# Optimization experiments

Measured on AMD Instinct MI355X. Metric: run time of the kernel, lower is better.

The kernel has to match this reference:

```python
import jax, jax.numpy as jnp
from jax import lax
import numpy as np

# dims
N = 8192        # words in sentence
LMAX = 16       # max chars per word (padded)
WED = 506       # word embedding dim
WHD = 512       # word LSTM hidden (input = WED + CHD = 512)
CED = 6         # char embedding dim
CHD = 6         # char LSTM hidden (hardcoded 6 in original)
WV = 50000      # word vocab
CV = 128        # char vocab
T = 64          # tagset size


def setup_inputs() -> dict:
    key = jax.random.key(0)
    ks = jax.random.split(key, 14)
    s = 0.1
    nrm = lambda k, shp: (jax.random.normal(k, shp, dtype=jnp.float32) * s)
    return {
        "sentence_words": jax.random.randint(ks[0], (N,), 0, WV),
        "sentence_characters": jax.random.randint(ks[1], (N, LMAX), 0, CV),
        "char_lengths": jax.random.randint(ks[2], (N,), 1, LMAX + 1),
        "word_emb": nrm(ks[3], (WV, WED)),
        "char_emb": nrm(ks[4], (CV, CED)),
        # PyTorch LSTM gate order: i, f, g, o. b = b_ih + b_hh combined.
        "c_Wih": nrm(ks[5], (4 * CHD, CED)),
        "c_Whh": nrm(ks[6], (4 * CHD, CHD)),
        "c_b": nrm(ks[7], (4 * CHD,)),
        "w_Wih": nrm(ks[8], (4 * WHD, WED + CHD)),
        "w_Whh": nrm(ks[9], (4 * WHD, WHD)),
        "w_b": nrm(ks[10], (4 * WHD,)),
        "out_W": nrm(ks[11], (T, WHD)),
        "out_b": nrm(ks[12], (T,)),
    }


def _gates(pre, c_prev):
    i, f, g, o = jnp.split(pre, 4, axis=-1)
    i = jax.nn.sigmoid(i)
    f = jax.nn.sigmoid(f)
    g = jnp.tanh(g)
    o = jax.nn.sigmoid(o)
    c_new = f * c_prev + i * g
    h_new = o * jnp.tanh(c_new)
    return h_new, c_new


def reference(sentence_words, sentence_characters, char_lengths,
              word_emb, char_emb, c_Wih, c_Whh, c_b,
              w_Wih, w_Whh, w_b, out_W, out_b):
    # ---- char-level LSTM: all words batched, masked by length ----
    ce = char_emb[sentence_characters]                  # [N, LMAX, CED]
    xproj = jnp.einsum('nlc,gc->nlg', ce, c_Wih) + c_b  # [N, LMAX, 4*CHD]
    xproj_t = jnp.swapaxes(xproj, 0, 1)                 # [LMAX, N, 4*CHD]
    mask_t = (jnp.arange(LMAX)[:, None] < char_lengths[None, :])[..., None]  # [LMAX, N, 1]

    def char_step(carry, xm):
        h, c = carry
        xp, m = xm
        h_new, c_new = _gates(xp + h @ c_Whh.T, c)
        return (jnp.where(m, h_new, h), jnp.where(m, c_new, c)), None

    z = jnp.zeros((N, CHD), dtype=xproj.dtype)
    (h_char, _), _ = lax.scan(char_step, (z, z), (xproj_t, mask_t))  # [N, CHD]

    # ---- word-level LSTM over the sentence (batch = 1) ----
    we = word_emb[sentence_words]                       # [N, WED]
    x = jnp.concatenate([we, h_char], axis=1)           # [N, WED+CHD]
    xp = x @ w_Wih.T + w_b                              # [N, 4*WHD]

    def word_step(carry, xt):
        h, c = carry
        h_new, c_new = _gates(xt + h @ w_Whh.T, c)
        return (h_new, c_new), h_new

    zw = jnp.zeros((WHD,), dtype=xp.dtype)
    _, hs = lax.scan(word_step, (zw, zw), xp)           # [N, WHD]

    logits = hs @ out_W.T + out_b                       # [N, T]
    return jax.nn.log_softmax(logits, axis=1)
```

## Files before the change

### kernel.cpp

```cpp
#include <hip/hip_runtime.h>
#include <hip/hip_bf16.h>
#include <math.h>

#define N_WORDS 8192
#define LMAX    16
#define WED     506
#define WHD     512
#define CED     6
#define CHD     6
#define CVOC    128
#define TAG     64
#define XDIM    512
#define G4      2048
#define NWG     64

__device__ __forceinline__ float fast_sigmoid(float x) { return 1.0f / (1.0f + __expf(-x)); }
__device__ __forceinline__ float fast_tanh(float x)    { return 2.0f / (1.0f + __expf(-2.0f * x)) - 1.0f; }

__global__ void __launch_bounds__(256) char_lstm_kernel(
    const int*   __restrict__ chars,
    const int*   __restrict__ lens,
    const float* __restrict__ char_emb,
    const float* __restrict__ cWih,
    const float* __restrict__ cWhh,
    const float* __restrict__ cb,
    float*       __restrict__ h_char)
{
    __shared__ float sWih[24][6], sWhh[24][6], sb[24], semb[CVOC][CED];
    int t = threadIdx.x;
    if (t < 144) { sWih[t / 6][t % 6] = cWih[t]; sWhh[t / 6][t % 6] = cWhh[t]; }
    if (t < 24) sb[t] = cb[t];
    for (int i = t; i < CVOC * CED; i += 256) semb[i / CED][i % CED] = char_emb[i];
    __syncthreads();

    int n = blockIdx.x * 256 + t;
    if (n >= N_WORDS) return;
    int len = lens[n];
    float h[CHD] = {0, 0, 0, 0, 0, 0};
    float c[CHD] = {0, 0, 0, 0, 0, 0};
    for (int l = 0; l < LMAX; ++l) {
        if (l >= len) break;
        int ch = chars[n * LMAX + l];
        float e[CED];
        #pragma unroll
        for (int k = 0; k < CED; ++k) e[k] = semb[ch][k];
        float pre[24];
        #pragma unroll
        for (int g = 0; g < 24; ++g) {
            float a = sb[g];
            #pragma unroll
            for (int k = 0; k < CED; ++k) a += e[k] * sWih[g][k];
            #pragma unroll
            for (int k = 0; k < CHD; ++k) a += h[k] * sWhh[g][k];
            pre[g] = a;
        }
        #pragma unroll
        for (int u = 0; u < CHD; ++u) {
            float ig = fast_sigmoid(pre[u]);
            float fg = fast_sigmoid(pre[6 + u]);
            float gg = fast_tanh(pre[12 + u]);
            float og = fast_sigmoid(pre[18 + u]);
            float cn = fg * c[u] + ig * gg;
            c[u] = cn;
            h[u] = og * fast_tanh(cn);
        }
    }
    for (int u = 0; u < CHD; ++u) h_char[n * CHD + u] = h[u];
}

__global__ void __launch_bounds__(256) build_x_kernel(
    const int*   __restrict__ words,
    const float* __restrict__ word_emb,
    const float* __restrict__ h_char,
    float*       __restrict__ X)
{
    long idx = (long)blockIdx.x * 256 + threadIdx.x;
    if (idx >= (long)N_WORDS * XDIM) return;
    int n = (int)(idx >> 9), k = (int)(idx & 511);
    float v;
    if (k < WED) v = word_emb[(long)words[n] * WED + k];
    else         v = h_char[n * CHD + (k - WED)];
    X[idx] = v;
}

#define BM 64
#define BN 64
#define BK 16
__global__ void __launch_bounds__(256) xp_gemm_kernel(
    const float* __restrict__ X,
    const float* __restrict__ Wih,
    const float* __restrict__ wb,
    float*       __restrict__ XP4)
{
    __shared__ float As[BM][BK + 1];
    __shared__ float Bs[BN][BK + 1];
    int tid = threadIdx.x;
    int bm = (blockIdx.x % (N_WORDS / BM)) * BM;
    int bn = (blockIdx.x / (N_WORDS / BM)) * BN;
    int ty = tid / 16, tx = tid % 16;
    float acc[4][4] = {};
    for (int k0 = 0; k0 < XDIM; k0 += BK) {
        #pragma unroll
        for (int i = 0; i < 4; ++i) {
            int e = tid + i * 256;
            int r = e >> 4, cc = e & 15;
            As[r][cc] = X[(long)(bm + r) * XDIM + k0 + cc];
            Bs[r][cc] = Wih[(long)(bn + r) * XDIM + k0 + cc];
        }
        __syncthreads();
        #pragma unroll
        for (int kk = 0; kk < BK; ++kk) {
            float a[4], b[4];
            #pragma unroll
            for (int i = 0; i < 4; ++i) a[i] = As[ty * 4 + i][kk];
            #pragma unroll
            for (int j = 0; j < 4; ++j) b[j] = Bs[tx * 4 + j][kk];
            #pragma unroll
            for (int i = 0; i < 4; ++i)
                #pragma unroll
                for (int j = 0; j < 4; ++j) acc[i][j] += a[i] * b[j];
        }
        __syncthreads();
    }
    #pragma unroll
    for (int i = 0; i < 4; ++i) {
        int m = bm + ty * 4 + i;
        #pragma unroll
        for (int j = 0; j < 4; ++j) {
            int g = bn + tx * 4 + j;
            int unit = g & 511, gate = g >> 9;
            XP4[((long)m * WHD + unit) * 4 + gate] = acc[i][j] + wb[g];
        }
    }
}

__global__ void __launch_bounds__(256, 1) word_lstm_kernel(
    const float* __restrict__ Whh,
    const float* __restrict__ XP4,
    float*       HS)
{
    __shared__ float hbuf[WHD];

    const int tid = threadIdx.x;
    const int wg  = blockIdx.x;
    const int ug  = tid >> 5;
    const int p   = tid & 31;
    const int j   = wg * 8 + ug;

    float w[4][16];
    #pragma unroll
    for (int r = 0; r < 4; ++r) {
        const float* src = Whh + (long)(r * 512 + j) * WHD + p;
        #pragma unroll
        for (int kk = 0; kk < 16; ++kk) w[r][kk] = src[kk * 32];
    }

    float c = 0.0f;
    float h16[16];
    #pragma unroll
    for (int kk = 0; kk < 16; ++kk) h16[kk] = 0.0f;

    for (int t = 0; t < N_WORDS; ++t) {
        const float4 xp = *(const float4*)(XP4 + ((long)t * WHD + j) * 4);

        if (t > 0) {
            if (tid < 64) {
                const unsigned long long* hrow =
                    (const unsigned long long*)(HS + (long)(t - 1) * WHD);
                float lo[4], hi[4];
                bool ready = false;
                while (!ready) {
                    unsigned long long q[4];
                    #pragma unroll
                    for (int i = 0; i < 4; ++i)
                        q[i] = __hip_atomic_load(&hrow[i * 64 + tid], __ATOMIC_RELAXED,
                                                 __HIP_MEMORY_SCOPE_AGENT);
                    ready = true;
                    #pragma unroll
                    for (int i = 0; i < 4; ++i) {
                        lo[i] = __uint_as_float((unsigned)(q[i] & 0xffffffffu));
                        hi[i] = __uint_as_float((unsigned)(q[i] >> 32));
                        ready = ready && (lo[i] > 0.5f) && (hi[i] > 0.5f);
                    }
                }
                #pragma unroll
                for (int i = 0; i < 4; ++i) {
                    hbuf[i * 128 + 2 * tid]     = lo[i] - 2.0f;
                    hbuf[i * 128 + 2 * tid + 1] = hi[i] - 2.0f;
                }
            }
            __syncthreads();
            #pragma unroll
            for (int kk = 0; kk < 16; ++kk) h16[kk] = hbuf[p + 32 * kk];
        }

        float di = 0, df = 0, dg = 0, dq = 0;
        #pragma unroll
        for (int kk = 0; kk < 16; ++kk) {
            di = fmaf(w[0][kk], h16[kk], di);
            df = fmaf(w[1][kk], h16[kk], df);
            dg = fmaf(w[2][kk], h16[kk], dg);
            dq = fmaf(w[3][kk], h16[kk], dq);
        }
        #pragma unroll
        for (int m = 16; m >= 1; m >>= 1) {
            di += __shfl_xor(di, m);
            df += __shfl_xor(df, m);
            dg += __shfl_xor(dg, m);
            dq += __shfl_xor(dq, m);
        }
        float ig = fast_sigmoid(xp.x + di);
        float fg = fast_sigmoid(xp.y + df);
        float gg = fast_tanh(xp.z + dg);
        float og = fast_sigmoid(xp.w + dq);
        c = fg * c + ig * gg;
        float hn = og * fast_tanh(c);

        if (p == 0)
            __hip_atomic_store(&HS[(long)t * WHD + j], hn + 2.0f, __ATOMIC_RELAXED,
                               __HIP_MEMORY_SCOPE_AGENT);
    }
}

__global__ void __launch_bounds__(256) transpose_outw_kernel(
    const float* __restrict__ outW, float* __restrict__ outWT)
{
    int e = blockIdx.x * 256 + threadIdx.x;
    if (e >= TAG * WHD) return;
    int g = e >> 9, k = e & 511;
    outWT[k * TAG + g] = outW[e];
}

__global__ void __launch_bounds__(64) logits_kernel(
    const float* __restrict__ HS,
    const float* __restrict__ outWT,
    const float* __restrict__ outb,
    float*       __restrict__ out)
{
    int n = blockIdx.x;
    int g = threadIdx.x;
    const float* hrow = HS + (long)n * WHD;
    float acc = outb[g];
    #pragma unroll 8
    for (int k = 0; k < WHD; ++k) acc += (hrow[k] - 2.0f) * outWT[k * TAG + g];
    float m = acc;
    #pragma unroll
    for (int s = 32; s >= 1; s >>= 1) m = fmaxf(m, __shfl_xor(m, s));
    float ex = __expf(acc - m);
    float ssum = ex;
    #pragma unroll
    for (int s = 32; s >= 1; s >>= 1) ssum += __shfl_xor(ssum, s);
    out[(long)n * TAG + g] = acc - m - logf(ssum);
}

extern "C" void kernel_launch(void* const* d_in, const int* in_sizes, int n_in,
                              void* d_out, int out_size, void* d_ws, size_t ws_size,
                              hipStream_t stream)
{
    const int*   words = (const int*)   d_in[0];
    const int*   chars = (const int*)   d_in[1];
    const int*   lens  = (const int*)   d_in[2];
    const float* wemb  = (const float*) d_in[3];
    const float* cemb  = (const float*) d_in[4];
    const float* cWih  = (const float*) d_in[5];
    const float* cWhh  = (const float*) d_in[6];
    const float* cb    = (const float*) d_in[7];
    const float* wWih  = (const float*) d_in[8];
    const float* wWhh  = (const float*) d_in[9];
    const float* wb    = (const float*) d_in[10];
    const float* outW  = (const float*) d_in[11];
    const float* outb  = (const float*) d_in[12];
    float* out = (float*)d_out;

    char* ws = (char*)d_ws;
    size_t off = 0;
    float* h_char = (float*)(ws + off); off += (size_t)N_WORDS * CHD * 4;
    float* X      = (float*)(ws + off); off += (size_t)N_WORDS * XDIM * 4;
    float* XP4    = (float*)(ws + off); off += (size_t)N_WORDS * G4 * 4;
    float* HS     = (float*)(ws + off); off += (size_t)N_WORDS * WHD * 4;
    float* outWT  = (float*)(ws + off); off += (size_t)WHD * TAG * 4;

    hipMemsetAsync(HS, 0, (size_t)N_WORDS * WHD * sizeof(float), stream);

    char_lstm_kernel<<<N_WORDS / 256, 256, 0, stream>>>(chars, lens, cemb, cWih, cWhh, cb, h_char);
    build_x_kernel<<<(N_WORDS * XDIM) / 256, 256, 0, stream>>>(words, wemb, h_char, X);
    xp_gemm_kernel<<<(N_WORDS / BM) * (G4 / BN), 256, 0, stream>>>(X, wWih, wb, XP4);
    transpose_outw_kernel<<<(TAG * WHD) / 256, 256, 0, stream>>>(outW, outWT);
    word_lstm_kernel<<<NWG, 256, 0, stream>>>(wWhh, XP4, HS);
    logits_kernel<<<N_WORDS, 64, 0, stream>>>(HS, outWT, outb, out);
}
```

Before: 18.06 ms.

## Split word LSTM into single-wave blocks that poll hidden state directly

```diff
diff --git a/kernel.cpp b/kernel.cpp
--- a/kernel.cpp
+++ b/kernel.cpp
@@ -12,7 +12,6 @@
 #define TAG     64
 #define XDIM    512
 #define G4      2048
-#define NWG     64
 
 __device__ __forceinline__ float fast_sigmoid(float x) { return 1.0f / (1.0f + __expf(-x)); }
 __device__ __forceinline__ float fast_tanh(float x)    { return 2.0f / (1.0f + __expf(-2.0f * x)) - 1.0f; }
@@ -134,25 +133,25 @@
     }
 }
 
-__global__ void __launch_bounds__(256, 1) word_lstm_kernel(
+__global__ void __launch_bounds__(64, 1) word_lstm_kernel(
     const float* __restrict__ Whh,
     const float* __restrict__ XP4,
     float*       HS)
 {
-    __shared__ float hbuf[WHD];
-
-    const int tid = threadIdx.x;
-    const int wg  = blockIdx.x;
-    const int ug  = tid >> 5;
-    const int p   = tid & 31;
-    const int j   = wg * 8 + ug;
+    const int lane = threadIdx.x;
+    const int p    = lane & 31;
+    const int j    = (blockIdx.x << 1) + (lane >> 5);
 
     float w[4][16];
     #pragma unroll
     for (int r = 0; r < 4; ++r) {
-        const float* src = Whh + (long)(r * 512 + j) * WHD + p;
-        #pragma unroll
-        for (int kk = 0; kk < 16; ++kk) w[r][kk] = src[kk * 32];
+        const float* src = Whh + (long)(r * 512 + j) * WHD + 2 * p;
+        #pragma unroll
+        for (int i = 0; i < 8; ++i) {
+            float2 v = *(const float2*)(src + 64 * i);
+            w[r][2 * i]     = v.x;
+            w[r][2 * i + 1] = v.y;
+        }
     }
 
     float c = 0.0f;
@@ -160,38 +159,37 @@
     #pragma unroll
     for (int kk = 0; kk < 16; ++kk) h16[kk] = 0.0f;
 
+    float4 xp = *(const float4*)(XP4 + (long)j * 4);
+
     for (int t = 0; t < N_WORDS; ++t) {
-        const float4 xp = *(const float4*)(XP4 + ((long)t * WHD + j) * 4);
+        float4 xp_next = xp;
+        if (t + 1 < N_WORDS)
+            xp_next = *(const float4*)(XP4 + ((long)(t + 1) * WHD + j) * 4);
 
         if (t > 0) {
-            if (tid < 64) {
-                const unsigned long long* hrow =
-                    (const unsigned long long*)(HS + (long)(t - 1) * WHD);
-                float lo[4], hi[4];
-                bool ready = false;
-                while (!ready) {
-                    unsigned long long q[4];
-                    #pragma unroll
-                    for (int i = 0; i < 4; ++i)
-                        q[i] = __hip_atomic_load(&hrow[i * 64 + tid], __ATOMIC_RELAXED,
-                                                 __HIP_MEMORY_SCOPE_AGENT);
-                    ready = true;
-                    #pragma unroll
-                    for (int i = 0; i < 4; ++i) {
-                        lo[i] = __uint_as_float((unsigned)(q[i] & 0xffffffffu));
-                        hi[i] = __uint_as_float((unsigned)(q[i] >> 32));
-                        ready = ready && (lo[i] > 0.5f) && (hi[i] > 0.5f);
-                    }
-                }
+            const unsigned long long* hrow =
+                (const unsigned long long*)(HS + (long)(t - 1) * WHD);
+            float lo[8], hi[8];
+            bool ready = false;
+            while (!ready) {
+                unsigned long long q[8];
                 #pragma unroll
-                for (int i = 0; i < 4; ++i) {
-                    hbuf[i * 128 + 2 * tid]     = lo[i] - 2.0f;
-                    hbuf[i * 128 + 2 * tid + 1] = hi[i] - 2.0f;
+                for (int i = 0; i < 8; ++i)
+                    q[i] = __hip_atomic_load(&hrow[i * 32 + p], __ATOMIC_RELAXED,
+                                             __HIP_MEMORY_SCOPE_AGENT);
+                ready = true;
+                #pragma unroll
+                for (int i = 0; i < 8; ++i) {
+                    lo[i] = __uint_as_float((unsigned)(q[i] & 0xffffffffu));
+                    hi[i] = __uint_as_float((unsigned)(q[i] >> 32));
+                    ready = ready && (lo[i] > 0.5f) && (hi[i] > 0.5f);
                 }
             }
-            __syncthreads();
-            #pragma unroll
-            for (int kk = 0; kk < 16; ++kk) h16[kk] = hbuf[p + 32 * kk];
+            #pragma unroll
+            for (int i = 0; i < 8; ++i) {
+                h16[2 * i]     = lo[i] - 2.0f;
+                h16[2 * i + 1] = hi[i] - 2.0f;
+            }
         }
 
         float di = 0, df = 0, dg = 0, dq = 0;
@@ -219,6 +217,7 @@
         if (p == 0)
             __hip_atomic_store(&HS[(long)t * WHD + j], hn + 2.0f, __ATOMIC_RELAXED,
                                __HIP_MEMORY_SCOPE_AGENT);
+        xp = xp_next;
     }
 }
 
@@ -286,6 +285,6 @@
     build_x_kernel<<<(N_WORDS * XDIM) / 256, 256, 0, stream>>>(words, wemb, h_char, X);
     xp_gemm_kernel<<<(N_WORDS / BM) * (G4 / BN), 256, 0, stream>>>(X, wWih, wb, XP4);
     transpose_outw_kernel<<<(TAG * WHD) / 256, 256, 0, stream>>>(outW, outWT);
-    word_lstm_kernel<<<NWG, 256, 0, stream>>>(wWhh, XP4, HS);
+    word_lstm_kernel<<<256, 64, 0, stream>>>(wWhh, XP4, HS);
     logits_kernel<<<N_WORDS, 64, 0, stream>>>(HS, outWT, outb, out);
 }
```

Result: slower. 22.07 ms (+22.2%).

## Confine word-LSTM recurrence to one XCD with role election and cache-hinted polling

Applied to the files above, without the earlier changes.

```diff
diff --git a/kernel.cpp b/kernel.cpp
--- a/kernel.cpp
+++ b/kernel.cpp
@@ -12,10 +12,18 @@
 #define TAG     64
 #define XDIM    512
 #define G4      2048
-#define NWG     64
+#define NBLK    256
+#define NROLE   32
 
 __device__ __forceinline__ float fast_sigmoid(float x) { return 1.0f / (1.0f + __expf(-x)); }
 __device__ __forceinline__ float fast_tanh(float x)    { return 2.0f / (1.0f + __expf(-2.0f * x)) - 1.0f; }
+
+__device__ __forceinline__ float q_lo(unsigned long long q) {
+    return __uint_as_float((unsigned)(q & 0xffffffffu));
+}
+__device__ __forceinline__ float q_hi(unsigned long long q) {
+    return __uint_as_float((unsigned)(q >> 32));
+}
 
 __global__ void __launch_bounds__(256) char_lstm_kernel(
     const int*   __restrict__ chars,
@@ -134,18 +142,46 @@
     }
 }
 
-__global__ void __launch_bounds__(256, 1) word_lstm_kernel(
+__global__ void __launch_bounds__(512, 1) word_lstm_kernel(
     const float* __restrict__ Whh,
     const float* __restrict__ XP4,
-    float*       HS)
+    float*       HS,
+    unsigned*    CTL)
 {
     __shared__ float hbuf[WHD];
+    __shared__ int s_role;
 
     const int tid = threadIdx.x;
-    const int wg  = blockIdx.x;
-    const int ug  = tid >> 5;
-    const int p   = tid & 31;
-    const int j   = wg * 8 + ug;
+
+    if (tid == 0) {
+        unsigned xcc;
+        asm volatile("s_getreg_b32 %0, hwreg(HW_REG_XCC_ID)" : "=s"(xcc));
+        xcc &= 7u;
+        __hip_atomic_fetch_add(&CTL[1 + xcc], 1u, __ATOMIC_RELAXED, __HIP_MEMORY_SCOPE_AGENT);
+        __hip_atomic_fetch_add(&CTL[0], 1u, __ATOMIC_RELAXED, __HIP_MEMORY_SCOPE_AGENT);
+        while (__hip_atomic_load(&CTL[0], __ATOMIC_RELAXED, __HIP_MEMORY_SCOPE_AGENT) < NBLK)
+            __builtin_amdgcn_s_sleep(1);
+        unsigned best = 0, bc = 0;
+        for (int i = 0; i < 8; ++i) {
+            unsigned cnum = __hip_atomic_load(&CTL[1 + i], __ATOMIC_RELAXED,
+                                              __HIP_MEMORY_SCOPE_AGENT);
+            if (cnum > bc) { bc = cnum; best = (unsigned)i; }
+        }
+        int role = -1;
+        if (xcc == best) {
+            unsigned s = __hip_atomic_fetch_add(&CTL[9], 1u, __ATOMIC_RELAXED,
+                                                __HIP_MEMORY_SCOPE_AGENT);
+            if (s < NROLE) role = (int)s;
+        }
+        s_role = role;
+    }
+    __syncthreads();
+    const int role = s_role;
+    if (role < 0) return;
+
+    const int ug = tid >> 5;
+    const int p  = tid & 31;
+    const int j  = role * 16 + ug;
 
     float w[4][16];
     #pragma unroll
@@ -167,21 +203,38 @@
             if (tid < 64) {
                 const unsigned long long* hrow =
                     (const unsigned long long*)(HS + (long)(t - 1) * WHD);
+                const unsigned long long* a0 = hrow + tid;
+                const unsigned long long* a1 = hrow + 64 + tid;
+                const unsigned long long* a2 = hrow + 128 + tid;
+                const unsigned long long* a3 = hrow + 192 + tid;
                 float lo[4], hi[4];
-                bool ready = false;
-                while (!ready) {
+                int it = 0;
+                for (;;) {
                     unsigned long long q[4];
-                    #pragma unroll
-                    for (int i = 0; i < 4; ++i)
-                        q[i] = __hip_atomic_load(&hrow[i * 64 + tid], __ATOMIC_RELAXED,
-                                                 __HIP_MEMORY_SCOPE_AGENT);
-                    ready = true;
+                    if ((++it & 7) != 0) {
+                        asm volatile(
+                            "global_load_dwordx2 %0, %4, off sc0\n\t"
+                            "global_load_dwordx2 %1, %5, off sc0\n\t"
+                            "global_load_dwordx2 %2, %6, off sc0\n\t"
+                            "global_load_dwordx2 %3, %7, off sc0\n\t"
+                            "s_waitcnt vmcnt(0)"
+                            : "=&v"(q[0]), "=&v"(q[1]), "=&v"(q[2]), "=&v"(q[3])
+                            : "v"(a0), "v"(a1), "v"(a2), "v"(a3)
+                            : "memory");
+                    } else {
+                        q[0] = __hip_atomic_load(a0, __ATOMIC_RELAXED, __HIP_MEMORY_SCOPE_AGENT);
+                        q[1] = __hip_atomic_load(a1, __ATOMIC_RELAXED, __HIP_MEMORY_SCOPE_AGENT);
+                        q[2] = __hip_atomic_load(a2, __ATOMIC_RELAXED, __HIP_MEMORY_SCOPE_AGENT);
+                        q[3] = __hip_atomic_load(a3, __ATOMIC_RELAXED, __HIP_MEMORY_SCOPE_AGENT);
+                    }
+                    bool ready = true;
                     #pragma unroll
                     for (int i = 0; i < 4; ++i) {
-                        lo[i] = __uint_as_float((unsigned)(q[i] & 0xffffffffu));
-                        hi[i] = __uint_as_float((unsigned)(q[i] >> 32));
+                        lo[i] = q_lo(q[i]);
+                        hi[i] = q_hi(q[i]);
                         ready = ready && (lo[i] > 0.5f) && (hi[i] > 0.5f);
                     }
+                    if (ready) break;
                 }
                 #pragma unroll
                 for (int i = 0; i < 4; ++i) {
@@ -216,9 +269,14 @@
         c = fg * c + ig * gg;
         float hn = og * fast_tanh(c);
 
-        if (p == 0)
-            __hip_atomic_store(&HS[(long)t * WHD + j], hn + 2.0f, __ATOMIC_RELAXED,
-                               __HIP_MEMORY_SCOPE_AGENT);
+        {
+            float  hv = hn + 2.0f;
+            float* hp = HS + (long)t * WHD + j;
+            if (p == 0)
+                asm volatile("global_store_dword %0, %1, off sc0" :: "v"(hp), "v"(hv) : "memory");
+            else if (p == 1)
+                asm volatile("global_store_dword %0, %1, off sc1" :: "v"(hp), "v"(hv) : "memory");
+        }
     }
 }
 
@@ -274,18 +332,20 @@
 
     char* ws = (char*)d_ws;
     size_t off = 0;
-    float* h_char = (float*)(ws + off); off += (size_t)N_WORDS * CHD * 4;
-    float* X      = (float*)(ws + off); off += (size_t)N_WORDS * XDIM * 4;
-    float* XP4    = (float*)(ws + off); off += (size_t)N_WORDS * G4 * 4;
-    float* HS     = (float*)(ws + off); off += (size_t)N_WORDS * WHD * 4;
-    float* outWT  = (float*)(ws + off); off += (size_t)WHD * TAG * 4;
+    float*    h_char = (float*)(ws + off); off += (size_t)N_WORDS * CHD * 4;
+    float*    X      = (float*)(ws + off); off += (size_t)N_WORDS * XDIM * 4;
+    float*    XP4    = (float*)(ws + off); off += (size_t)N_WORDS * G4 * 4;
+    float*    HS     = (float*)(ws + off); off += (size_t)N_WORDS * WHD * 4;
+    float*    outWT  = (float*)(ws + off); off += (size_t)WHD * TAG * 4;
+    unsigned* CTL    = (unsigned*)(ws + off); off += 16 * sizeof(unsigned);
 
     hipMemsetAsync(HS, 0, (size_t)N_WORDS * WHD * sizeof(float), stream);
+    hipMemsetAsync(CTL, 0, 16 * sizeof(unsigned), stream);
 
     char_lstm_kernel<<<N_WORDS / 256, 256, 0, stream>>>(chars, lens, cemb, cWih, cWhh, cb, h_char);
     build_x_kernel<<<(N_WORDS * XDIM) / 256, 256, 0, stream>>>(words, wemb, h_char, X);
     xp_gemm_kernel<<<(N_WORDS / BM) * (G4 / BN), 256, 0, stream>>>(X, wWih, wb, XP4);
     transpose_outw_kernel<<<(TAG * WHD) / 256, 256, 0, stream>>>(outW, outWT);
-    word_lstm_kernel<<<NWG, 256, 0, stream>>>(wWhh, XP4, HS);
+    word_lstm_kernel<<<NBLK, 512, 0, stream>>>(wWhh, XP4, HS, CTL);
     logits_kernel<<<N_WORDS, 64, 0, stream>>>(HS, outWT, outb, out);
 }
```

New measurement: 43.22 ms. +139.3%, slower.
